# Optimization experiments

Measured on AMD Instinct MI355X. Metric: run time of the kernel, lower is better.

## Reference

```python
import jax, jax.numpy as jnp
import numpy as np


def setup_inputs() -> dict:
    key = jax.random.key(0)
    k1, k2 = jax.random.split(key)
    B, L1, L2, D = 64, 1024, 1024, 768
    sent = jax.random.normal(k1, (B, L1, D), dtype=jnp.float32)
    e = jax.random.normal(k2, (B, L2, L1), dtype=jnp.float32)
    return {"sent": sent, "e": e}


def reference(sent, e):
    # Stable softmax over last axis (alignment weights over L1),
    # then weighted pooling of sent: equivalent to es @ sent.
    es = jax.nn.softmax(e, axis=-1)              # [B, L2, L1]
    out = jnp.einsum('bql,bld->bqd', es, sent)   # [B, L2, D]
    return out
```

## Files before the change

kernel.cpp:

```cpp
#include <hip/hip_runtime.h>
#include <hip/hip_bf16.h>


#define B_  64
#define L1_ 1024
#define L2_ 1024
#define D_  768

typedef __attribute__((ext_vector_type(8))) short short8;
typedef __attribute__((ext_vector_type(4))) float f32x4;
typedef __attribute__((ext_vector_type(8))) unsigned short ushort8;

static __device__ __forceinline__ unsigned short f2bf(float x) {
  union { float f; unsigned int u; } c; c.f = x;
  unsigned int r = c.u + 0x7FFF + ((c.u >> 16) & 1);
  return (unsigned short)(r >> 16);
}

__global__ __launch_bounds__(256) void transpose_cast_kernel(const float* __restrict__ sent,
                                                             unsigned short* __restrict__ sT) {
  __shared__ unsigned short tile[64][66];
  const int b  = blockIdx.z;
  const int l0 = blockIdx.y << 6;
  const int d0 = blockIdx.x << 6;
  const int t  = threadIdx.x;
  const float* sp = sent + ((size_t)b * L1_ + l0) * D_ + d0;
  const int c4 = (t & 15) << 2;
  const int r0 = t >> 4;
#pragma unroll
  for (int p = 0; p < 4; ++p) {
    const int r = r0 + (p << 4);
    float4 v = *reinterpret_cast<const float4*>(sp + (size_t)r * D_ + c4);
    tile[r][c4 + 0] = f2bf(v.x);
    tile[r][c4 + 1] = f2bf(v.y);
    tile[r][c4 + 2] = f2bf(v.z);
    tile[r][c4 + 3] = f2bf(v.w);
  }
  __syncthreads();
  unsigned short* op = sT + ((size_t)b * D_ + d0) * L1_ + l0;
  const int l8  = (t & 7) << 3;
  const int dd0 = t >> 3;
#pragma unroll
  for (int p = 0; p < 2; ++p) {
    const int d = dd0 + (p << 5);
    ushort8 w;
#pragma unroll
    for (int j = 0; j < 8; ++j) w[j] = tile[l8 + j][d];
    *reinterpret_cast<ushort8*>(op + (size_t)d * L1_ + l8) = w;
  }
}

#define BM 128
#define BN 256
#define BK 32
#define NT    (L1_ / BK)
#define NTILE (D_ / BN)
#define MTILE (L2_ / BM)
#define NWG   (NTILE * MTILE * B_)

#define SW(r) ((((r) >> 2) ^ (r)) & 3)

#define GLOAD(gp, lp) \
  __builtin_amdgcn_global_load_lds((const __attribute__((address_space(1))) char*)(gp), \
                                   (__attribute__((address_space(3))) char*)(lp), 16, 0, 0)

#define LOADA(T) do { if ((T) < NT) {                                           \
    aregs[0] = *reinterpret_cast<const float4*>(Ae + (size_t)rA * L1_ + (T) * BK + cA);     \
    aregs[1] = *reinterpret_cast<const float4*>(Ae + (size_t)rA * L1_ + (T) * BK + cA + 4); \
  } } while (0)

#define EXPWRITE(T) do { if ((T) < NT) {                                        \
    unsigned short* Ad_ = &As[(T) % 3][0];                                      \
    float ex_[8];                                                               \
    ex_[0] = __expf(aregs[0].x); ex_[1] = __expf(aregs[0].y);                   \
    ex_[2] = __expf(aregs[0].z); ex_[3] = __expf(aregs[0].w);                   \
    ex_[4] = __expf(aregs[1].x); ex_[5] = __expf(aregs[1].y);                   \
    ex_[6] = __expf(aregs[1].z); ex_[7] = __expf(aregs[1].w);                   \
    psum += ((ex_[0] + ex_[1]) + (ex_[2] + ex_[3]))                             \
          + ((ex_[4] + ex_[5]) + (ex_[6] + ex_[7]));                            \
    ushort8 w0_;                                                                \
    _Pragma("unroll")                                                           \
    for (int q_ = 0; q_ < 8; ++q_) w0_[q_] = f2bf(ex_[q_]);                     \
    *reinterpret_cast<ushort8*>(&Ad_[rA * BK + aslot * 8]) = w0_;               \
  } } while (0)

#define SB(T) do { if ((T) < NT) {                                              \
    GLOAD(Bb + (size_t)rB0 * L1_ + (T) * BK + sB0, &Bs[(T) % 3][(w * 32) * BK]);      \
    GLOAD(Bb + (size_t)rB1 * L1_ + (T) * BK + sB1, &Bs[(T) % 3][(w * 32 + 16) * BK]); \
  } } while (0)

__global__ __launch_bounds__(512, 2) void gemm_kernel(const float* __restrict__ e,
                                                      const unsigned short* __restrict__ sT,
                                                      float* __restrict__ out) {
  __shared__ __align__(16) unsigned short As[3][BM * BK];
  __shared__ __align__(16) unsigned short Bs[3][BN * BK];
  __shared__ float sArr[BM];

  const int orig = blockIdx.x;
  const int wgid = (orig & 7) * (NWG / 8) + (orig >> 3);
  const int b    = wgid / (NTILE * MTILE);
  const int rem  = wgid % (NTILE * MTILE);
  const int m0   = (rem / NTILE) * BM;
  const int n0   = (rem % NTILE) * BN;

  const int t    = threadIdx.x;
  const int lane = t & 63;
  const int w    = t >> 6;
  const int wm   = w >> 2;
  const int wn   = w & 3;
  const int l15  = lane & 15;
  const int ksl  = lane >> 4;
  const int rA   = w * 16 + (lane >> 2);
  const int cA   = (lane & 3) * 8;
  const int aslot = (lane & 3) ^ SW(rA);
  const int rB0  = w * 32 + (lane >> 2);
  const int rB1  = rB0 + 16;
  const int sB0  = ((lane & 3) ^ SW(rB0)) * 8;
  const int sB1  = ((lane & 3) ^ SW(rB1)) * 8;

  const float*          Ae = e  + ((size_t)b * L2_ + m0) * L1_;
  const unsigned short* Bb = sT + ((size_t)b * D_  + n0) * L1_;

  f32x4 acc[4][4] = {};
  float4 aregs[2];
  float psum = 0.f;

  LOADA(0);
  SB(0); SB(1);
  EXPWRITE(0);
  LOADA(1);
  asm volatile("s_waitcnt vmcnt(4) lgkmcnt(0)" ::: "memory");
  __builtin_amdgcn_s_barrier();
  __builtin_amdgcn_sched_barrier(0);

  for (int kt = 0; kt < NT; ++kt) {
    SB(kt + 2);
    EXPWRITE(kt + 1);
    LOADA(kt + 2);

    const unsigned short* Apt = As[kt % 3];
    const unsigned short* Bpt = Bs[kt % 3];
    short8 a[4], bb[4];
    __builtin_amdgcn_s_setprio(1);
#pragma unroll
    for (int i = 0; i < 4; ++i) {
      const int ra = wm * 64 + i * 16 + l15;
      a[i] = *reinterpret_cast<const short8*>(&Apt[ra * BK + ((ksl ^ SW(ra)) << 3)]);
      const int rb = wn * 64 + i * 16 + l15;
      bb[i] = *reinterpret_cast<const short8*>(&Bpt[rb * BK + ((ksl ^ SW(rb)) << 3)]);
    }
#pragma unroll
    for (int i = 0; i < 4; ++i)
#pragma unroll
      for (int jn = 0; jn < 4; ++jn)
        acc[i][jn] = __builtin_amdgcn_mfma_f32_16x16x32_bf16(a[i], bb[jn], acc[i][jn], 0, 0, 0);
    __builtin_amdgcn_s_setprio(0);

    if (kt < NT - 1) {
      asm volatile("s_waitcnt lgkmcnt(0)" ::: "memory");
      __builtin_amdgcn_s_barrier();
      __builtin_amdgcn_sched_barrier(0);
    }
  }

  psum += __shfl_xor(psum, 1);
  psum += __shfl_xor(psum, 2);
  if ((lane & 3) == 0) sArr[rA] = psum;
  __syncthreads();

  const int rbase = (lane >> 4) << 2;
  float* Cb = out + ((size_t)b * L2_ + m0 + wm * 64) * D_ + n0 + wn * 64;
#pragma unroll
  for (int i = 0; i < 4; ++i) {
    float inv[4];
#pragma unroll
    for (int r = 0; r < 4; ++r)
      inv[r] = 1.0f / sArr[wm * 64 + i * 16 + rbase + r];
#pragma unroll
    for (int jn = 0; jn < 4; ++jn)
#pragma unroll
      for (int r = 0; r < 4; ++r)
        Cb[(size_t)(i * 16 + rbase + r) * D_ + jn * 16 + l15] = acc[i][jn][r] * inv[r];
  }
}

extern "C" void kernel_launch(void* const* d_in, const int* in_sizes, int n_in,
                              void* d_out, int out_size, void* d_ws, size_t ws_size,
                              hipStream_t stream) {
  const float* sent = (const float*)d_in[0];
  const float* e    = (const float*)d_in[1];
  float* out = (float*)d_out;

  unsigned short* sT = (unsigned short*)d_ws;

  transpose_cast_kernel<<<dim3(D_ / 64, L1_ / 64, B_), 256, 0, stream>>>(sent, sT);
  gemm_kernel<<<dim3(NWG), 512, 0, stream>>>(e, sT, out);
}
```

Measured before the change: 252.5 us.

## Enlarge GEMM tile to 256x256x64 with phased ping-pong pipeline

Doubles the M tile and K step and moves from a triple-buffered to a double-buffered LDS pipeline. Each K tile is split into four phases that interleave the B prefetch, the A exp/convert/write and the next A global load with the MFMA work. An 8-way XOR swizzle is used for the wider K slice. The aim is more MFMA work per global load and better overlap of the softmax exp with the matrix math, at the cost of twice the accumulators, more A registers held per thread, more barriers per tile and possible lower occupancy or register spills.

Measured after the change: 739.7 us. +192.9%, slower.

```diff
diff --git a/kernel.cpp b/kernel.cpp
--- a/kernel.cpp
+++ b/kernel.cpp
@@ -50,58 +50,103 @@
   }
 }
 
-#define BM 128
+#define BM 256
 #define BN 256
-#define BK 32
+#define BK 64
 #define NT    (L1_ / BK)
-#define NTILE (D_ / BN)
-#define MTILE (L2_ / BM)
-#define NWG   (NTILE * MTILE * B_)
-
-#define SW(r) ((((r) >> 2) ^ (r)) & 3)
+#define MT    (L2_ / BM)
+#define NTL   (D_ / BN)
+#define NWG   (B_ * MT * NTL)
 
 #define GLOAD(gp, lp) \
   __builtin_amdgcn_global_load_lds((const __attribute__((address_space(1))) char*)(gp), \
                                    (__attribute__((address_space(3))) char*)(lp), 16, 0, 0)
 
-#define LOADA(T) do { if ((T) < NT) {                                           \
-    aregs[0] = *reinterpret_cast<const float4*>(Ae + (size_t)rA * L1_ + (T) * BK + cA);     \
-    aregs[1] = *reinterpret_cast<const float4*>(Ae + (size_t)rA * L1_ + (T) * BK + cA + 4); \
+#define SBST(T, BUF) do { \
+    const int _tb = (T) & (NT - 1); \
+    _Pragma("unroll") \
+    for (int c_ = 0; c_ < 4; ++c_) \
+      GLOAD(Bsrc + (size_t)c_ * 64 * L1_ + _tb * BK, &Bs[BUF][(c_ * 64 + w * 8) * BK]); \
+  } while (0)
+
+#define LOADA(T) do { \
+    const int _ta = (T) & (NT - 1); \
+    _Pragma("unroll") \
+    for (int j_ = 0; j_ < 8; ++j_) \
+      ar[j_] = *reinterpret_cast<const float4*>(Asrc + _ta * BK + j_ * 4); \
+  } while (0)
+
+#define EXPWRITE(VALID, BUF) do { if (VALID) { \
+    _Pragma("unroll") \
+    for (int q_ = 0; q_ < 4; ++q_) { \
+      float ex_[8]; \
+      ex_[0] = __expf(ar[2 * q_].x);     ex_[1] = __expf(ar[2 * q_].y); \
+      ex_[2] = __expf(ar[2 * q_].z);     ex_[3] = __expf(ar[2 * q_].w); \
+      ex_[4] = __expf(ar[2 * q_ + 1].x); ex_[5] = __expf(ar[2 * q_ + 1].y); \
+      ex_[6] = __expf(ar[2 * q_ + 1].z); ex_[7] = __expf(ar[2 * q_ + 1].w); \
+      psum += ((ex_[0] + ex_[1]) + (ex_[2] + ex_[3])) \
+            + ((ex_[4] + ex_[5]) + (ex_[6] + ex_[7])); \
+      ushort8 wv_; \
+      _Pragma("unroll") \
+      for (int m_ = 0; m_ < 8; ++m_) wv_[m_] = f2bf(ex_[m_]); \
+      *reinterpret_cast<ushort8*>(&As[BUF][rA * BK + (((kh * 4 + q_) ^ (rA & 7)) << 3)]) = wv_; \
+    } \
   } } while (0)
 
-#define EXPWRITE(T) do { if ((T) < NT) {                                        \
-    unsigned short* Ad_ = &As[(T) % 3][0];                                      \
-    float ex_[8];                                                               \
-    ex_[0] = __expf(aregs[0].x); ex_[1] = __expf(aregs[0].y);                   \
-    ex_[2] = __expf(aregs[0].z); ex_[3] = __expf(aregs[0].w);                   \
-    ex_[4] = __expf(aregs[1].x); ex_[5] = __expf(aregs[1].y);                   \
-    ex_[6] = __expf(aregs[1].z); ex_[7] = __expf(aregs[1].w);                   \
-    psum += ((ex_[0] + ex_[1]) + (ex_[2] + ex_[3]))                             \
-          + ((ex_[4] + ex_[5]) + (ex_[6] + ex_[7]));                            \
-    ushort8 w0_;                                                                \
-    _Pragma("unroll")                                                           \
-    for (int q_ = 0; q_ < 8; ++q_) w0_[q_] = f2bf(ex_[q_]);                     \
-    *reinterpret_cast<ushort8*>(&Ad_[rA * BK + aslot * 8]) = w0_;               \
-  } } while (0)
-
-#define SB(T) do { if ((T) < NT) {                                              \
-    GLOAD(Bb + (size_t)rB0 * L1_ + (T) * BK + sB0, &Bs[(T) % 3][(w * 32) * BK]);      \
-    GLOAD(Bb + (size_t)rB1 * L1_ + (T) * BK + sB1, &Bs[(T) % 3][(w * 32 + 16) * BK]); \
-  } } while (0)
+#define PHASE(RB, RH, KH, ...) do { \
+    __VA_ARGS__ \
+    short8 a_[4], b_[4]; \
+    _Pragma("unroll") \
+    for (int ii = 0; ii < 4; ++ii) { \
+      const int ra_ = wm * 128 + ((RH) * 4 + ii) * 16 + l15; \
+      a_[ii] = *reinterpret_cast<const short8*>( \
+          &As[RB][ra_ * BK + ((((KH) * 4 + ksl) ^ (l15 & 7)) << 3)]); \
+      const int rb_ = wn * 64 + ii * 16 + l15; \
+      b_[ii] = *reinterpret_cast<const short8*>( \
+          &Bs[RB][rb_ * BK + ((((KH) * 4 + ksl) ^ (l15 & 7)) << 3)]); \
+    } \
+    __builtin_amdgcn_sched_barrier(0); \
+    __builtin_amdgcn_s_barrier(); \
+    asm volatile("s_waitcnt lgkmcnt(0)" ::: "memory"); \
+    __builtin_amdgcn_sched_barrier(0); \
+    __builtin_amdgcn_s_setprio(1); \
+    _Pragma("unroll") \
+    for (int ii = 0; ii < 4; ++ii) \
+      _Pragma("unroll") \
+      for (int jj = 0; jj < 4; ++jj) \
+        acc[(RH) * 4 + ii][jj] = __builtin_amdgcn_mfma_f32_16x16x32_bf16( \
+            a_[ii], b_[jj], acc[(RH) * 4 + ii][jj], 0, 0, 0); \
+    __builtin_amdgcn_s_setprio(0); \
+    __builtin_amdgcn_sched_barrier(0); \
+    __builtin_amdgcn_s_barrier(); \
+  } while (0)
+
+#define TILE(T, RB, SBUF) do { \
+    PHASE(RB, 0, 0, SBST((T) + 1, SBUF); ); \
+    PHASE(RB, 0, 1, ; ); \
+    PHASE(RB, 1, 0, \
+        asm volatile("s_waitcnt vmcnt(4)" ::: "memory"); \
+        __builtin_amdgcn_sched_barrier(0); \
+        EXPWRITE((T) + 1 < NT, SBUF); ); \
+    PHASE(RB, 1, 1, \
+        LOADA((T) + 2); \
+        asm volatile("s_waitcnt vmcnt(8)" ::: "memory"); \
+        __builtin_amdgcn_sched_barrier(0); ); \
+  } while (0)
 
 __global__ __launch_bounds__(512, 2) void gemm_kernel(const float* __restrict__ e,
                                                       const unsigned short* __restrict__ sT,
                                                       float* __restrict__ out) {
-  __shared__ __align__(16) unsigned short As[3][BM * BK];
-  __shared__ __align__(16) unsigned short Bs[3][BN * BK];
+  __shared__ __align__(16) unsigned short As[2][BM * BK];
+  __shared__ __align__(16) unsigned short Bs[2][BN * BK];
   __shared__ float sArr[BM];
 
   const int orig = blockIdx.x;
   const int wgid = (orig & 7) * (NWG / 8) + (orig >> 3);
-  const int b    = wgid / (NTILE * MTILE);
-  const int rem  = wgid % (NTILE * MTILE);
-  const int m0   = (rem / NTILE) * BM;
-  const int n0   = (rem % NTILE) * BN;
+  const int b    = wgid / (MT * NTL);
+  const int rem  = wgid % (MT * NTL);
+  const int m0   = (rem / NTL) * BM;
+  const int n0   = (rem % NTL) * BN;
 
   const int t    = threadIdx.x;
   const int lane = t & 63;
@@ -110,77 +155,53 @@
   const int wn   = w & 3;
   const int l15  = lane & 15;
   const int ksl  = lane >> 4;
-  const int rA   = w * 16 + (lane >> 2);
-  const int cA   = (lane & 3) * 8;
-  const int aslot = (lane & 3) ^ SW(rA);
-  const int rB0  = w * 32 + (lane >> 2);
-  const int rB1  = rB0 + 16;
-  const int sB0  = ((lane & 3) ^ SW(rB0)) * 8;
-  const int sB1  = ((lane & 3) ^ SW(rB1)) * 8;
-
-  const float*          Ae = e  + ((size_t)b * L2_ + m0) * L1_;
-  const unsigned short* Bb = sT + ((size_t)b * D_  + n0) * L1_;
-
-  f32x4 acc[4][4] = {};
-  float4 aregs[2];
+
+  const int rA = t >> 1;
+  const int kh = t & 1;
+
+  const int brow  = lane >> 3;
+  const int bslot = (lane & 7) ^ brow;
+
+  const float*          Ae   = e  + ((size_t)b * L2_ + m0) * L1_;
+  const unsigned short* Bb   = sT + ((size_t)b * D_  + n0) * L1_;
+  const unsigned short* Bsrc = Bb + (size_t)(w * 8 + brow) * L1_ + bslot * 8;
+  const float*          Asrc = Ae + (size_t)rA * L1_ + kh * 32;
+
+  f32x4 acc[8][4] = {};
+  float4 ar[8];
   float psum = 0.f;
 
   LOADA(0);
-  SB(0); SB(1);
-  EXPWRITE(0);
+  SBST(0, 0);
+  EXPWRITE(1, 0);
   LOADA(1);
-  asm volatile("s_waitcnt vmcnt(4) lgkmcnt(0)" ::: "memory");
+  asm volatile("s_waitcnt vmcnt(8)" ::: "memory");
+  asm volatile("s_waitcnt lgkmcnt(0)" ::: "memory");
   __builtin_amdgcn_s_barrier();
-  __builtin_amdgcn_sched_barrier(0);
-
-  for (int kt = 0; kt < NT; ++kt) {
-    SB(kt + 2);
-    EXPWRITE(kt + 1);
-    LOADA(kt + 2);
-
-    const unsigned short* Apt = As[kt % 3];
-    const unsigned short* Bpt = Bs[kt % 3];
-    short8 a[4], bb[4];
-    __builtin_amdgcn_s_setprio(1);
-#pragma unroll
-    for (int i = 0; i < 4; ++i) {
-      const int ra = wm * 64 + i * 16 + l15;
-      a[i] = *reinterpret_cast<const short8*>(&Apt[ra * BK + ((ksl ^ SW(ra)) << 3)]);
-      const int rb = wn * 64 + i * 16 + l15;
-      bb[i] = *reinterpret_cast<const short8*>(&Bpt[rb * BK + ((ksl ^ SW(rb)) << 3)]);
-    }
-#pragma unroll
-    for (int i = 0; i < 4; ++i)
-#pragma unroll
-      for (int jn = 0; jn < 4; ++jn)
-        acc[i][jn] = __builtin_amdgcn_mfma_f32_16x16x32_bf16(a[i], bb[jn], acc[i][jn], 0, 0, 0);
-    __builtin_amdgcn_s_setprio(0);
-
-    if (kt < NT - 1) {
-      asm volatile("s_waitcnt lgkmcnt(0)" ::: "memory");
-      __builtin_amdgcn_s_barrier();
-      __builtin_amdgcn_sched_barrier(0);
-    }
+
+#pragma unroll
+  for (int kt = 0; kt < NT; kt += 2) {
+    TILE(kt,     0, 1);
+    TILE(kt + 1, 1, 0);
   }
 
   psum += __shfl_xor(psum, 1);
-  psum += __shfl_xor(psum, 2);
-  if ((lane & 3) == 0) sArr[rA] = psum;
+  if ((lane & 1) == 0) sArr[rA] = psum;
   __syncthreads();
 
   const int rbase = (lane >> 4) << 2;
-  float* Cb = out + ((size_t)b * L2_ + m0 + wm * 64) * D_ + n0 + wn * 64;
-#pragma unroll
-  for (int i = 0; i < 4; ++i) {
+  float* Cb = out + ((size_t)b * L2_ + m0 + wm * 128) * D_ + n0 + wn * 64;
+#pragma unroll
+  for (int i = 0; i < 8; ++i) {
     float inv[4];
 #pragma unroll
     for (int r = 0; r < 4; ++r)
-      inv[r] = 1.0f / sArr[wm * 64 + i * 16 + rbase + r];
-#pragma unroll
-    for (int jn = 0; jn < 4; ++jn)
+      inv[r] = 1.0f / sArr[wm * 128 + i * 16 + rbase + r];
+#pragma unroll
+    for (int jj = 0; jj < 4; ++jj)
 #pragma unroll
       for (int r = 0; r < 4; ++r)
-        Cb[(size_t)(i * 16 + rbase + r) * D_ + jn * 16 + l15] = acc[i][jn][r] * inv[r];
+        Cb[(size_t)(i * 16 + rbase + r) * D_ + jj * 16 + l15] = acc[i][jj][r] * inv[r];
   }
 }
 
```
